# Kernel optimization log

Hardware: AMD Instinct MI355X
Metric: run time of the kernel (lower is better)

## Reference

```python
import jax, jax.numpy as jnp
import numpy as np

N_NODES = 50000
N_EDGES = 800000
VOCAB = 800000
CONCEPT_DIM = 100
HIDDEN_DIM = 200
OUTPUT_DIM = 100


def setup_inputs() -> dict:
    key = jax.random.key(0)
    ks = jax.random.split(key, 8)
    cncpt_ids = jax.random.randint(ks[0], (N_NODES,), 0, VOCAB, dtype=jnp.int64 if jax.config.jax_enable_x64 else jnp.int32)
    edge_src = jax.random.randint(ks[1], (N_EDGES,), 0, N_NODES, dtype=jnp.int32)
    edge_dst = jax.random.randint(ks[2], (N_EDGES,), 0, N_NODES, dtype=jnp.int32)
    emb = jax.random.normal(ks[3], (VOCAB, CONCEPT_DIM), dtype=jnp.float32)
    W1 = jax.random.normal(ks[4], (CONCEPT_DIM, HIDDEN_DIM), dtype=jnp.float32) / np.sqrt(CONCEPT_DIM)
    b1 = jnp.zeros((HIDDEN_DIM,), dtype=jnp.float32)
    W2 = jax.random.normal(ks[5], (HIDDEN_DIM, OUTPUT_DIM), dtype=jnp.float32) / np.sqrt(HIDDEN_DIM)
    b2 = jnp.zeros((OUTPUT_DIM,), dtype=jnp.float32)
    return {"emb": emb, "W1": W1, "b1": b1, "W2": W2, "b2": b2,
            "cncpt_ids": cncpt_ids, "edge_src": edge_src, "edge_dst": edge_dst}


def _gcn_layer(h, edge_src, edge_dst, W, b):
    # DGL update_all(copy_src, sum): gather src features, scatter-add to dst
    msgs = h[edge_src]                                        # [E, d_in]
    agg = jax.ops.segment_sum(msgs, edge_dst, num_segments=N_NODES)  # [N, d_in]
    return jax.nn.relu(agg @ W + b)                           # [N, d_out]


def reference(emb, W1, b1, W2, b2, cncpt_ids, edge_src, edge_dst):
    h = emb[cncpt_ids]                                        # [N, concept_dim]
    h = _gcn_layer(h, edge_src, edge_dst, W1, b1)             # [N, hidden]
    h = _gcn_layer(h, edge_src, edge_dst, W2, b2)             # [N, output]
    return h
```

## Files before the change

kernel.cpp:

```cpp
#include <hip/hip_runtime.h>

#define N_NODES 50000
#define N_EDGES 800000
#define CDIM 100
#define HDIM 200
#define ODIM 100

#define PITCH_U 64

typedef __bf16 bf16x8 __attribute__((ext_vector_type(8)));
typedef float f32x4 __attribute__((ext_vector_type(4)));
typedef unsigned short ushort_t;

__device__ __forceinline__ unsigned f2bf(float f) {
    unsigned u = __float_as_uint(f);
    u = (u + 0x7FFFu + ((u >> 16) & 1u)) >> 16;
    return u;
}
__device__ __forceinline__ float bflo(unsigned u) { return __uint_as_float(u << 16); }
__device__ __forceinline__ float bfhi(unsigned u) { return __uint_as_float(u & 0xFFFF0000u); }


__global__ void count_rank(const int* __restrict__ dst, int* __restrict__ deg,
                           int* __restrict__ rank) {
    int e = blockIdx.x * 256 + threadIdx.x;
    if (e < N_EDGES) rank[e] = atomicAdd(&deg[dst[e]], 1);
}

__global__ __launch_bounds__(1024) void scan_deg(const int* __restrict__ deg,
                                                 int* __restrict__ off) {
    const int T = 1024;
    const int PER = 52;
    int t = threadIdx.x;
    int start = t * PER;
    const int4* deg4 = (const int4*)deg;

    int sum = 0;
    if (start + PER <= N_NODES) {
#pragma unroll
        for (int q = 0; q < PER / 4; ++q) {
            int4 v = deg4[start / 4 + q];
            sum += v.x + v.y + v.z + v.w;
        }
    } else {
        for (int i = start; i < N_NODES; ++i) sum += deg[i];
    }

    __shared__ int ls[T];
    ls[t] = sum;
    __syncthreads();
    for (int o = 1; o < T; o <<= 1) {
        int v = (t >= o) ? ls[t - o] : 0;
        __syncthreads();
        ls[t] += v;
        __syncthreads();
    }
    int run = (t == 0) ? 0 : ls[t - 1];

    if (start + PER <= N_NODES) {
        int4* off4 = (int4*)off;
#pragma unroll
        for (int q = 0; q < PER / 4; ++q) {
            int4 v = deg4[start / 4 + q];
            int4 o;
            o.x = run;
            o.y = o.x + v.x;
            o.z = o.y + v.y;
            o.w = o.z + v.z;
            run = o.w + v.w;
            off4[start / 4 + q] = o;
        }
    } else if (start <= N_NODES) {
        for (int i = start; i < N_NODES; ++i) {
            off[i] = run;
            run += deg[i];
        }
        off[N_NODES] = run;
    }
}


__global__ __launch_bounds__(256) void scatter_gather_prep(
    const int* __restrict__ esrc, const int* __restrict__ edst,
    const int* __restrict__ off, const int* __restrict__ rank, int* __restrict__ ssrc,
    const float4* __restrict__ emb, const int* __restrict__ ids, uint2* __restrict__ h0,
    const float* __restrict__ W1, const float* __restrict__ W2,
    ushort_t* __restrict__ W1t, ushort_t* __restrict__ W2t) {
    int b = blockIdx.x;
    if (b < 3125) {
        int e = b * 256 + threadIdx.x;
        if (e < N_EDGES) {
            int p = off[edst[e]] + rank[e];
            ssrc[p] = esrc[e];
        }
    } else if (b < 9375) {
        int i = (b - 3125) * 256 + threadIdx.x;
        const int TOT = N_NODES * 32;
        if (i < TOT) {
            int n = i >> 5, q = i & 31;
            uint2 o = make_uint2(0u, 0u);
            if (q < 25) {
                float4 v = emb[(size_t)ids[n] * 25 + q];
                o.x = f2bf(v.x) | (f2bf(v.y) << 16);
                o.y = f2bf(v.z) | (f2bf(v.w) << 16);
            }
            h0[i] = o;
        }
    } else {
        int i = (b - 9375) * 256 + threadIdx.x;
        if (i < 208 * 128) {
            int n = i >> 7, k = i & 127;
            float v = (n < HDIM && k < CDIM) ? W1[k * HDIM + n] : 0.f;
            W1t[i] = (ushort_t)f2bf(v);
        } else {
            int j = i - 208 * 128;
            if (j < 112 * 256) {
                int n = j >> 8, k = j & 255;
                float v = (n < ODIM && k < HDIM) ? W2[k * ODIM + n] : 0.f;
                W2t[j] = (ushort_t)f2bf(v);
            }
        }
    }
}


template <bool BIAS_RELU>
__global__ __launch_bounds__(256) void agg_bf16(const unsigned* __restrict__ hb,
                                                const int* __restrict__ ssrc,
                                                const int* __restrict__ off,
                                                const float* __restrict__ bias,
                                                unsigned* __restrict__ outb,
                                                float2* __restrict__ outf) {
    int wave = threadIdx.x >> 6;
    int lane = threadIdx.x & 63;
    int n = blockIdx.x * 4 + wave;
    if (n >= N_NODES) return;
    int s0 = off[n], s1 = off[n + 1];

    float2 a0 = {0.f, 0.f}, a1 = {0.f, 0.f}, a2 = {0.f, 0.f}, a3 = {0.f, 0.f};
    int j = s0;
    for (; j + 7 < s1; j += 8) {
        int r0 = ssrc[j],     r1 = ssrc[j + 1], r2 = ssrc[j + 2], r3 = ssrc[j + 3];
        int r4 = ssrc[j + 4], r5 = ssrc[j + 5], r6 = ssrc[j + 6], r7 = ssrc[j + 7];
        unsigned u0 = hb[(size_t)r0 * PITCH_U + lane];
        unsigned u1 = hb[(size_t)r1 * PITCH_U + lane];
        unsigned u2 = hb[(size_t)r2 * PITCH_U + lane];
        unsigned u3 = hb[(size_t)r3 * PITCH_U + lane];
        unsigned u4 = hb[(size_t)r4 * PITCH_U + lane];
        unsigned u5 = hb[(size_t)r5 * PITCH_U + lane];
        unsigned u6 = hb[(size_t)r6 * PITCH_U + lane];
        unsigned u7 = hb[(size_t)r7 * PITCH_U + lane];
        a0.x += bflo(u0); a0.y += bfhi(u0);
        a1.x += bflo(u1); a1.y += bfhi(u1);
        a2.x += bflo(u2); a2.y += bfhi(u2);
        a3.x += bflo(u3); a3.y += bfhi(u3);
        a0.x += bflo(u4); a0.y += bfhi(u4);
        a1.x += bflo(u5); a1.y += bfhi(u5);
        a2.x += bflo(u6); a2.y += bfhi(u6);
        a3.x += bflo(u7); a3.y += bfhi(u7);
    }
    for (; j + 3 < s1; j += 4) {
        int r0 = ssrc[j], r1 = ssrc[j + 1], r2 = ssrc[j + 2], r3 = ssrc[j + 3];
        unsigned u0 = hb[(size_t)r0 * PITCH_U + lane];
        unsigned u1 = hb[(size_t)r1 * PITCH_U + lane];
        unsigned u2 = hb[(size_t)r2 * PITCH_U + lane];
        unsigned u3 = hb[(size_t)r3 * PITCH_U + lane];
        a0.x += bflo(u0); a0.y += bfhi(u0);
        a1.x += bflo(u1); a1.y += bfhi(u1);
        a2.x += bflo(u2); a2.y += bfhi(u2);
        a3.x += bflo(u3); a3.y += bfhi(u3);
    }
    {
        int rem = s1 - j;
        if (rem > 0) { unsigned u = hb[(size_t)ssrc[j] * PITCH_U + lane];     a0.x += bflo(u); a0.y += bfhi(u); }
        if (rem > 1) { unsigned u = hb[(size_t)ssrc[j + 1] * PITCH_U + lane]; a1.x += bflo(u); a1.y += bfhi(u); }
        if (rem > 2) { unsigned u = hb[(size_t)ssrc[j + 2] * PITCH_U + lane]; a2.x += bflo(u); a2.y += bfhi(u); }
    }
    float rx = (a0.x + a1.x) + (a2.x + a3.x);
    float ry = (a0.y + a1.y) + (a2.y + a3.y);
    if (BIAS_RELU) {
        if (lane < 50) {
            rx = fmaxf(rx + bias[2 * lane], 0.f);
            ry = fmaxf(ry + bias[2 * lane + 1], 0.f);
            outf[(size_t)n * 50 + lane] = make_float2(rx, ry);
        }
    } else {
        outb[(size_t)n * PITCH_U + lane] = f2bf(rx) | (f2bf(ry) << 16);
    }
}


__global__ __launch_bounds__(256) void gemm_fused(const ushort_t* __restrict__ Ab,
                                                  const ushort_t* __restrict__ W1t,
                                                  const float* __restrict__ b1,
                                                  const ushort_t* __restrict__ W2t,
                                                  ushort_t* __restrict__ gb) {
    const int P2 = 264;
    __shared__ alignas(16) ushort_t H1s[64 * P2];

    int tid = threadIdx.x, lane = tid & 63, w = tid >> 6;
    int rl = lane & 15, kg = lane >> 4;
    int row0 = blockIdx.x * 64;

    size_t abase = ((size_t)(row0 + w * 16 + rl)) * 128;
    f32x4 acc1[13];
#pragma unroll
    for (int t = 0; t < 13; ++t) acc1[t] = (f32x4){0.f, 0.f, 0.f, 0.f};
#pragma unroll
    for (int k2 = 0; k2 < 4; ++k2) {
        bf16x8 a = *reinterpret_cast<const bf16x8*>(&Ab[abase + k2 * 32 + kg * 8]);
#pragma unroll
        for (int t = 0; t < 13; ++t) {
            bf16x8 b = *reinterpret_cast<const bf16x8*>(&W1t[(t * 16 + rl) * 128 + k2 * 32 + kg * 8]);
            acc1[t] = __builtin_amdgcn_mfma_f32_16x16x32_bf16(a, b, acc1[t], 0, 0, 0);
        }
    }
    for (int idx = tid; idx < 64 * 32; idx += 256) {
        int r = idx >> 5, c = idx & 31;
        ((unsigned*)&H1s[r * P2 + 200])[c] = 0;
    }
#pragma unroll
    for (int t = 0; t < 13; ++t) {
        int col = t * 16 + rl;
        if (col < HDIM) {
            float bv = b1[col];
#pragma unroll
            for (int i = 0; i < 4; ++i) {
                int r = w * 16 + kg * 4 + i;
                H1s[r * P2 + col] = (ushort_t)f2bf(fmaxf(acc1[t][i] + bv, 0.f));
            }
        }
    }
    __syncthreads();

    f32x4 acc2[7];
#pragma unroll
    for (int t = 0; t < 7; ++t) acc2[t] = (f32x4){0.f, 0.f, 0.f, 0.f};
#pragma unroll
    for (int k2 = 0; k2 < 8; ++k2) {
        bf16x8 a = *reinterpret_cast<const bf16x8*>(&H1s[(w * 16 + rl) * P2 + k2 * 32 + kg * 8]);
#pragma unroll
        for (int t = 0; t < 7; ++t) {
            bf16x8 b = *reinterpret_cast<const bf16x8*>(&W2t[(t * 16 + rl) * 256 + k2 * 32 + kg * 8]);
            acc2[t] = __builtin_amdgcn_mfma_f32_16x16x32_bf16(a, b, acc2[t], 0, 0, 0);
        }
    }

#pragma unroll
    for (int t = 0; t < 7; ++t) {
        int col = t * 16 + rl;
#pragma unroll
        for (int i = 0; i < 4; ++i) {
            int row = row0 + w * 16 + kg * 4 + i;
            if (row < N_NODES) {
                float v = (col < ODIM) ? acc2[t][i] : 0.f;
                gb[(size_t)row * 128 + col] = (ushort_t)f2bf(v);
            }
        }
    }
    unsigned* gbu = (unsigned*)gb;
    for (int idx = tid; idx < 64 * 8; idx += 256) {
        int r = idx >> 3, c = idx & 7;
        int row = row0 + r;
        if (row < N_NODES) gbu[(size_t)row * PITCH_U + 56 + c] = 0;
    }
}


extern "C" void kernel_launch(void* const* d_in, const int* in_sizes, int n_in,
                              void* d_out, int out_size, void* d_ws, size_t ws_size,
                              hipStream_t stream) {
    const float4* emb = (const float4*)d_in[0];
    const float* W1  = (const float*)d_in[1];
    const float* b1  = (const float*)d_in[2];
    const float* W2  = (const float*)d_in[3];
    const float* b2  = (const float*)d_in[4];
    const int* ids   = (const int*)d_in[5];
    const int* esrc  = (const int*)d_in[6];
    const int* edst  = (const int*)d_in[7];
    float2* out = (float2*)d_out;

    unsigned* h0b = (unsigned*)d_ws;
    unsigned* a1b = h0b + (size_t)N_NODES * PITCH_U;
    unsigned* gbu = a1b + (size_t)N_NODES * PITCH_U;
    ushort_t* W1t = (ushort_t*)(gbu + (size_t)N_NODES * PITCH_U);
    ushort_t* W2t = W1t + 208 * 128;
    int* deg   = (int*)(W2t + 112 * 256);
    int* off   = deg + N_NODES;
    int* rank  = off + (N_NODES + 1);
    int* ssrc  = rank + N_EDGES;

    hipMemsetAsync(deg, 0, N_NODES * sizeof(int), stream);

    count_rank<<<(N_EDGES + 255) / 256, 256, 0, stream>>>(edst, deg, rank);
    scan_deg<<<1, 1024, 0, stream>>>(deg, off);

    scatter_gather_prep<<<9591, 256, 0, stream>>>(esrc, edst, off, rank, ssrc,
                                                  emb, ids, (uint2*)h0b,
                                                  W1, W2, W1t, W2t);

    agg_bf16<false><<<N_NODES / 4, 256, 0, stream>>>(h0b, ssrc, off,
                                                     nullptr, a1b, nullptr);
    gemm_fused<<<(N_NODES + 63) / 64, 256, 0, stream>>>((const ushort_t*)a1b, W1t, b1,
                                                        W2t, (ushort_t*)gbu);
    agg_bf16<true><<<N_NODES / 4, 256, 0, stream>>>(gbu, ssrc, off,
                                                    b2, nullptr, out);
}
```

Before: 199.5 us.

## Fuse first-layer aggregation into the fused MLP GEMM kernel via shared memory

The first neighbor aggregation is moved into the GEMM kernel. Each 64-row block aggregates its own nodes into shared memory as bf16, then loads the A fragments from LDS instead of from a global intermediate buffer. This removes one kernel launch and the global write and read of the aggregated features. The cost is that each wave now aggregates 16 nodes one after another, which lowers the parallelism available to hide gather latency (782 blocks versus 12500 before) and may make the kernel latency-bound.

Result: slower. 259.8 us (+30.3%).

```diff
diff --git a/kernel.cpp b/kernel.cpp
--- a/kernel.cpp
+++ b/kernel.cpp
@@ -20,123 +20,10 @@
 __device__ __forceinline__ float bflo(unsigned u) { return __uint_as_float(u << 16); }
 __device__ __forceinline__ float bfhi(unsigned u) { return __uint_as_float(u & 0xFFFF0000u); }
 
-
-__global__ void count_rank(const int* __restrict__ dst, int* __restrict__ deg,
-                           int* __restrict__ rank) {
-    int e = blockIdx.x * 256 + threadIdx.x;
-    if (e < N_EDGES) rank[e] = atomicAdd(&deg[dst[e]], 1);
-}
-
-__global__ __launch_bounds__(1024) void scan_deg(const int* __restrict__ deg,
-                                                 int* __restrict__ off) {
-    const int T = 1024;
-    const int PER = 52;
-    int t = threadIdx.x;
-    int start = t * PER;
-    const int4* deg4 = (const int4*)deg;
-
-    int sum = 0;
-    if (start + PER <= N_NODES) {
-#pragma unroll
-        for (int q = 0; q < PER / 4; ++q) {
-            int4 v = deg4[start / 4 + q];
-            sum += v.x + v.y + v.z + v.w;
-        }
-    } else {
-        for (int i = start; i < N_NODES; ++i) sum += deg[i];
-    }
-
-    __shared__ int ls[T];
-    ls[t] = sum;
-    __syncthreads();
-    for (int o = 1; o < T; o <<= 1) {
-        int v = (t >= o) ? ls[t - o] : 0;
-        __syncthreads();
-        ls[t] += v;
-        __syncthreads();
-    }
-    int run = (t == 0) ? 0 : ls[t - 1];
-
-    if (start + PER <= N_NODES) {
-        int4* off4 = (int4*)off;
-#pragma unroll
-        for (int q = 0; q < PER / 4; ++q) {
-            int4 v = deg4[start / 4 + q];
-            int4 o;
-            o.x = run;
-            o.y = o.x + v.x;
-            o.z = o.y + v.y;
-            o.w = o.z + v.z;
-            run = o.w + v.w;
-            off4[start / 4 + q] = o;
-        }
-    } else if (start <= N_NODES) {
-        for (int i = start; i < N_NODES; ++i) {
-            off[i] = run;
-            run += deg[i];
-        }
-        off[N_NODES] = run;
-    }
-}
-
-
-__global__ __launch_bounds__(256) void scatter_gather_prep(
-    const int* __restrict__ esrc, const int* __restrict__ edst,
-    const int* __restrict__ off, const int* __restrict__ rank, int* __restrict__ ssrc,
-    const float4* __restrict__ emb, const int* __restrict__ ids, uint2* __restrict__ h0,
-    const float* __restrict__ W1, const float* __restrict__ W2,
-    ushort_t* __restrict__ W1t, ushort_t* __restrict__ W2t) {
-    int b = blockIdx.x;
-    if (b < 3125) {
-        int e = b * 256 + threadIdx.x;
-        if (e < N_EDGES) {
-            int p = off[edst[e]] + rank[e];
-            ssrc[p] = esrc[e];
-        }
-    } else if (b < 9375) {
-        int i = (b - 3125) * 256 + threadIdx.x;
-        const int TOT = N_NODES * 32;
-        if (i < TOT) {
-            int n = i >> 5, q = i & 31;
-            uint2 o = make_uint2(0u, 0u);
-            if (q < 25) {
-                float4 v = emb[(size_t)ids[n] * 25 + q];
-                o.x = f2bf(v.x) | (f2bf(v.y) << 16);
-                o.y = f2bf(v.z) | (f2bf(v.w) << 16);
-            }
-            h0[i] = o;
-        }
-    } else {
-        int i = (b - 9375) * 256 + threadIdx.x;
-        if (i < 208 * 128) {
-            int n = i >> 7, k = i & 127;
-            float v = (n < HDIM && k < CDIM) ? W1[k * HDIM + n] : 0.f;
-            W1t[i] = (ushort_t)f2bf(v);
-        } else {
-            int j = i - 208 * 128;
-            if (j < 112 * 256) {
-                int n = j >> 8, k = j & 255;
-                float v = (n < ODIM && k < HDIM) ? W2[k * ODIM + n] : 0.f;
-                W2t[j] = (ushort_t)f2bf(v);
-            }
-        }
-    }
-}
-
-
-template <bool BIAS_RELU>
-__global__ __launch_bounds__(256) void agg_bf16(const unsigned* __restrict__ hb,
-                                                const int* __restrict__ ssrc,
-                                                const int* __restrict__ off,
-                                                const float* __restrict__ bias,
-                                                unsigned* __restrict__ outb,
-                                                float2* __restrict__ outf) {
-    int wave = threadIdx.x >> 6;
-    int lane = threadIdx.x & 63;
-    int n = blockIdx.x * 4 + wave;
-    if (n >= N_NODES) return;
+__device__ __forceinline__ float2 agg_core(int n, int lane, const unsigned* __restrict__ hb,
+                                           const int* __restrict__ ssrc,
+                                           const int* __restrict__ off) {
     int s0 = off[n], s1 = off[n + 1];
-
     float2 a0 = {0.f, 0.f}, a1 = {0.f, 0.f}, a2 = {0.f, 0.f}, a3 = {0.f, 0.f};
     int j = s0;
     for (; j + 7 < s1; j += 8) {
@@ -176,48 +63,163 @@
         if (rem > 1) { unsigned u = hb[(size_t)ssrc[j + 1] * PITCH_U + lane]; a1.x += bflo(u); a1.y += bfhi(u); }
         if (rem > 2) { unsigned u = hb[(size_t)ssrc[j + 2] * PITCH_U + lane]; a2.x += bflo(u); a2.y += bfhi(u); }
     }
-    float rx = (a0.x + a1.x) + (a2.x + a3.x);
-    float ry = (a0.y + a1.y) + (a2.y + a3.y);
-    if (BIAS_RELU) {
-        if (lane < 50) {
-            rx = fmaxf(rx + bias[2 * lane], 0.f);
-            ry = fmaxf(ry + bias[2 * lane + 1], 0.f);
-            outf[(size_t)n * 50 + lane] = make_float2(rx, ry);
+    return make_float2((a0.x + a1.x) + (a2.x + a3.x), (a0.y + a1.y) + (a2.y + a3.y));
+}
+
+
+__global__ void count_rank(const int* __restrict__ dst, int* __restrict__ deg,
+                           int* __restrict__ rank) {
+    int e = blockIdx.x * 256 + threadIdx.x;
+    if (e < N_EDGES) rank[e] = atomicAdd(&deg[dst[e]], 1);
+}
+
+__global__ __launch_bounds__(1024) void scan_deg(const int* __restrict__ deg,
+                                                 int* __restrict__ off) {
+    const int T = 1024;
+    const int PER = 52;
+    int t = threadIdx.x;
+    int start = t * PER;
+    const int4* deg4 = (const int4*)deg;
+
+    int sum = 0;
+    if (start + PER <= N_NODES) {
+#pragma unroll
+        for (int q = 0; q < PER / 4; ++q) {
+            int4 v = deg4[start / 4 + q];
+            sum += v.x + v.y + v.z + v.w;
         }
     } else {
-        outb[(size_t)n * PITCH_U + lane] = f2bf(rx) | (f2bf(ry) << 16);
-    }
-}
-
-
-__global__ __launch_bounds__(256) void gemm_fused(const ushort_t* __restrict__ Ab,
-                                                  const ushort_t* __restrict__ W1t,
-                                                  const float* __restrict__ b1,
-                                                  const ushort_t* __restrict__ W2t,
-                                                  ushort_t* __restrict__ gb) {
+        for (int i = start; i < N_NODES; ++i) sum += deg[i];
+    }
+
+    __shared__ int ls[T];
+    ls[t] = sum;
+    __syncthreads();
+    for (int o = 1; o < T; o <<= 1) {
+        int v = (t >= o) ? ls[t - o] : 0;
+        __syncthreads();
+        ls[t] += v;
+        __syncthreads();
+    }
+    int run = (t == 0) ? 0 : ls[t - 1];
+
+    if (start + PER <= N_NODES) {
+        int4* off4 = (int4*)off;
+#pragma unroll
+        for (int q = 0; q < PER / 4; ++q) {
+            int4 v = deg4[start / 4 + q];
+            int4 o;
+            o.x = run;
+            o.y = o.x + v.x;
+            o.z = o.y + v.y;
+            o.w = o.z + v.z;
+            run = o.w + v.w;
+            off4[start / 4 + q] = o;
+        }
+    } else if (start <= N_NODES) {
+        for (int i = start; i < N_NODES; ++i) {
+            off[i] = run;
+            run += deg[i];
+        }
+        off[N_NODES] = run;
+    }
+}
+
+
+__global__ __launch_bounds__(256) void scatter_gather_prep(
+    const int* __restrict__ esrc, const int* __restrict__ edst,
+    const int* __restrict__ off, const int* __restrict__ rank, int* __restrict__ ssrc,
+    const float4* __restrict__ emb, const int* __restrict__ ids, uint2* __restrict__ h0,
+    const float* __restrict__ W1, const float* __restrict__ W2,
+    ushort_t* __restrict__ W1t, ushort_t* __restrict__ W2t) {
+    int b = blockIdx.x;
+    if (b < 3125) {
+        int e = b * 256 + threadIdx.x;
+        if (e < N_EDGES) {
+            int p = off[edst[e]] + rank[e];
+            ssrc[p] = esrc[e];
+        }
+    } else if (b < 9375) {
+        int i = (b - 3125) * 256 + threadIdx.x;
+        const int TOT = N_NODES * 32;
+        if (i < TOT) {
+            int n = i >> 5, q = i & 31;
+            uint2 o = make_uint2(0u, 0u);
+            if (q < 25) {
+                float4 v = emb[(size_t)ids[n] * 25 + q];
+                o.x = f2bf(v.x) | (f2bf(v.y) << 16);
+                o.y = f2bf(v.z) | (f2bf(v.w) << 16);
+            }
+            h0[i] = o;
+        }
+    } else {
+        int i = (b - 9375) * 256 + threadIdx.x;
+        if (i < 208 * 128) {
+            int n = i >> 7, k = i & 127;
+            float v = (n < HDIM && k < CDIM) ? W1[k * HDIM + n] : 0.f;
+            W1t[i] = (ushort_t)f2bf(v);
+        } else {
+            int j = i - 208 * 128;
+            if (j < 112 * 256) {
+                int n = j >> 8, k = j & 255;
+                float v = (n < ODIM && k < HDIM) ? W2[k * ODIM + n] : 0.f;
+                W2t[j] = (ushort_t)f2bf(v);
+            }
+        }
+    }
+}
+
+
+__global__ __launch_bounds__(256) void agg_mlp(const unsigned* __restrict__ hb,
+                                               const int* __restrict__ ssrc,
+                                               const int* __restrict__ off,
+                                               const ushort_t* __restrict__ W1t,
+                                               const float* __restrict__ b1,
+                                               const ushort_t* __restrict__ W2t,
+                                               ushort_t* __restrict__ gb) {
     const int P2 = 264;
-    __shared__ alignas(16) ushort_t H1s[64 * P2];
+    const int AP = 136;
+    __shared__ alignas(16) ushort_t smem[64 * P2];
+    unsigned* AsU = (unsigned*)smem;
+    ushort_t* As = smem;
+    ushort_t* H1s = smem;
 
     int tid = threadIdx.x, lane = tid & 63, w = tid >> 6;
     int rl = lane & 15, kg = lane >> 4;
     int row0 = blockIdx.x * 64;
 
-    size_t abase = ((size_t)(row0 + w * 16 + rl)) * 128;
-    f32x4 acc1[13];
-#pragma unroll
-    for (int t = 0; t < 13; ++t) acc1[t] = (f32x4){0.f, 0.f, 0.f, 0.f};
-#pragma unroll
-    for (int k2 = 0; k2 < 4; ++k2) {
-        bf16x8 a = *reinterpret_cast<const bf16x8*>(&Ab[abase + k2 * 32 + kg * 8]);
-#pragma unroll
-        for (int t = 0; t < 13; ++t) {
-            bf16x8 b = *reinterpret_cast<const bf16x8*>(&W1t[(t * 16 + rl) * 128 + k2 * 32 + kg * 8]);
-            acc1[t] = __builtin_amdgcn_mfma_f32_16x16x32_bf16(a, b, acc1[t], 0, 0, 0);
-        }
-    }
+#pragma unroll 1
+    for (int i = 0; i < 16; ++i) {
+        int l = w * 16 + i;
+        int n = row0 + l;
+        if (n < N_NODES) {
+            float2 r = agg_core(n, lane, hb, ssrc, off);
+            AsU[l * (AP / 2) + lane] = f2bf(r.x) | (f2bf(r.y) << 16);
+        }
+    }
+    __syncthreads();
+
+    bf16x8 afr[4];
+#pragma unroll
+    for (int k2 = 0; k2 < 4; ++k2)
+        afr[k2] = *reinterpret_cast<const bf16x8*>(&As[(w * 16 + rl) * AP + k2 * 32 + kg * 8]);
+    __syncthreads();
+
     for (int idx = tid; idx < 64 * 32; idx += 256) {
         int r = idx >> 5, c = idx & 31;
         ((unsigned*)&H1s[r * P2 + 200])[c] = 0;
+    }
+
+    f32x4 acc1[13];
+#pragma unroll
+    for (int t = 0; t < 13; ++t) acc1[t] = (f32x4){0.f, 0.f, 0.f, 0.f};
+#pragma unroll
+    for (int k2 = 0; k2 < 4; ++k2) {
+#pragma unroll
+        for (int t = 0; t < 13; ++t) {
+            bf16x8 b = *reinterpret_cast<const bf16x8*>(&W1t[(t * 16 + rl) * 128 + k2 * 32 + kg * 8]);
+            acc1[t] = __builtin_amdgcn_mfma_f32_16x16x32_bf16(afr[k2], b, acc1[t], 0, 0, 0);
+        }
     }
 #pragma unroll
     for (int t = 0; t < 13; ++t) {
@@ -263,6 +265,24 @@
         int r = idx >> 3, c = idx & 7;
         int row = row0 + r;
         if (row < N_NODES) gbu[(size_t)row * PITCH_U + 56 + c] = 0;
+    }
+}
+
+
+__global__ __launch_bounds__(256) void agg_out(const unsigned* __restrict__ hb,
+                                               const int* __restrict__ ssrc,
+                                               const int* __restrict__ off,
+                                               const float* __restrict__ bias,
+                                               float2* __restrict__ outf) {
+    int wave = threadIdx.x >> 6;
+    int lane = threadIdx.x & 63;
+    int n = blockIdx.x * 4 + wave;
+    if (n >= N_NODES) return;
+    float2 r = agg_core(n, lane, hb, ssrc, off);
+    if (lane < 50) {
+        float rx = fmaxf(r.x + bias[2 * lane], 0.f);
+        float ry = fmaxf(r.y + bias[2 * lane + 1], 0.f);
+        outf[(size_t)n * 50 + lane] = make_float2(rx, ry);
     }
 }
 
@@ -281,8 +301,7 @@
     float2* out = (float2*)d_out;
 
     unsigned* h0b = (unsigned*)d_ws;
-    unsigned* a1b = h0b + (size_t)N_NODES * PITCH_U;
-    unsigned* gbu = a1b + (size_t)N_NODES * PITCH_U;
+    unsigned* gbu = h0b + (size_t)N_NODES * PITCH_U;
     ushort_t* W1t = (ushort_t*)(gbu + (size_t)N_NODES * PITCH_U);
     ushort_t* W2t = W1t + 208 * 128;
     int* deg   = (int*)(W2t + 112 * 256);
@@ -299,10 +318,7 @@
                                                   emb, ids, (uint2*)h0b,
                                                   W1, W2, W1t, W2t);
 
-    agg_bf16<false><<<N_NODES / 4, 256, 0, stream>>>(h0b, ssrc, off,
-                                                     nullptr, a1b, nullptr);
-    gemm_fused<<<(N_NODES + 63) / 64, 256, 0, stream>>>((const ushort_t*)a1b, W1t, b1,
-                                                        W2t, (ushort_t*)gbu);
-    agg_bf16<true><<<N_NODES / 4, 256, 0, stream>>>(gbu, ssrc, off,
-                                                    b2, nullptr, out);
-}
+    agg_mlp<<<(N_NODES + 63) / 64, 256, 0, stream>>>(h0b, ssrc, off, W1t, b1, W2t,
+                                                     (ushort_t*)gbu);
+    agg_out<<<N_NODES / 4, 256, 0, stream>>>(gbu, ssrc, off, b2, out);
+}
```

## Split each aggregation wave into two half-waves gathering two edges with 8-byte loads

Applied to the files above, without the earlier changes.

The aggregation kernels now have each half of a 64-lane wave handle a different edge. Each lane loads a uint2 (four bf16 values) per row, so two neighbor rows are fetched per instruction, and the two halves are combined with a cross-lane shuffle. The edge-count atomics are folded into the embedding-gather and weight-prep kernel, and the edge scatter moves into its own kernel. The intermediate buffer is removed by reusing the h0 and gb buffers in ping-pong fashion. The goal is wider loads, more memory parallelism and fewer launches, at the cost of an extra shuffle reduction and half-idle lanes when a node's edge count is odd.

Result: slower. 205.0 us (+2.8%).

```diff
diff --git a/kernel.cpp b/kernel.cpp
--- a/kernel.cpp
+++ b/kernel.cpp
@@ -7,6 +7,7 @@
 #define ODIM 100
 
 #define PITCH_U 64
+#define PITCH_U2 32
 
 typedef __bf16 bf16x8 __attribute__((ext_vector_type(8)));
 typedef float f32x4 __attribute__((ext_vector_type(4)));
@@ -20,92 +21,82 @@
 __device__ __forceinline__ float bflo(unsigned u) { return __uint_as_float(u << 16); }
 __device__ __forceinline__ float bfhi(unsigned u) { return __uint_as_float(u & 0xFFFF0000u); }
 
-
-__global__ void count_rank(const int* __restrict__ dst, int* __restrict__ deg,
-                           int* __restrict__ rank) {
-    int e = blockIdx.x * 256 + threadIdx.x;
-    if (e < N_EDGES) rank[e] = atomicAdd(&deg[dst[e]], 1);
-}
-
-__global__ __launch_bounds__(1024) void scan_deg(const int* __restrict__ deg,
-                                                 int* __restrict__ off) {
-    const int T = 1024;
-    const int PER = 52;
-    int t = threadIdx.x;
-    int start = t * PER;
-    const int4* deg4 = (const int4*)deg;
-
-    int sum = 0;
-    if (start + PER <= N_NODES) {
-#pragma unroll
-        for (int q = 0; q < PER / 4; ++q) {
-            int4 v = deg4[start / 4 + q];
-            sum += v.x + v.y + v.z + v.w;
-        }
-    } else {
-        for (int i = start; i < N_NODES; ++i) sum += deg[i];
-    }
-
-    __shared__ int ls[T];
-    ls[t] = sum;
-    __syncthreads();
-    for (int o = 1; o < T; o <<= 1) {
-        int v = (t >= o) ? ls[t - o] : 0;
-        __syncthreads();
-        ls[t] += v;
-        __syncthreads();
-    }
-    int run = (t == 0) ? 0 : ls[t - 1];
-
-    if (start + PER <= N_NODES) {
-        int4* off4 = (int4*)off;
-#pragma unroll
-        for (int q = 0; q < PER / 4; ++q) {
-            int4 v = deg4[start / 4 + q];
-            int4 o;
-            o.x = run;
-            o.y = o.x + v.x;
-            o.z = o.y + v.y;
-            o.w = o.z + v.z;
-            run = o.w + v.w;
-            off4[start / 4 + q] = o;
-        }
-    } else if (start <= N_NODES) {
-        for (int i = start; i < N_NODES; ++i) {
-            off[i] = run;
-            run += deg[i];
-        }
-        off[N_NODES] = run;
-    }
-}
-
-
-__global__ __launch_bounds__(256) void scatter_gather_prep(
-    const int* __restrict__ esrc, const int* __restrict__ edst,
-    const int* __restrict__ off, const int* __restrict__ rank, int* __restrict__ ssrc,
+#define ACC4(a, u)                          \
+    do {                                    \
+        (a).x += bflo((u).x);               \
+        (a).y += bfhi((u).x);               \
+        (a).z += bflo((u).y);               \
+        (a).w += bfhi((u).y);               \
+    } while (0)
+
+
+__device__ __forceinline__ float4 agg_core2(int n, int lane, const uint2* __restrict__ hb2,
+                                            const int* __restrict__ ssrc,
+                                            const int* __restrict__ off) {
+    int s0 = off[n], s1 = off[n + 1];
+    int half = lane >> 5;
+    int li = lane & 31;
+    float4 a0 = {0.f, 0.f, 0.f, 0.f}, a1 = {0.f, 0.f, 0.f, 0.f};
+    float4 a2 = {0.f, 0.f, 0.f, 0.f}, a3 = {0.f, 0.f, 0.f, 0.f};
+    int j = s0;
+    for (; j + 7 < s1; j += 8) {
+        int i0 = ssrc[j + 0 + half];
+        int i1 = ssrc[j + 2 + half];
+        int i2 = ssrc[j + 4 + half];
+        int i3 = ssrc[j + 6 + half];
+        uint2 u0 = hb2[(size_t)i0 * PITCH_U2 + li];
+        uint2 u1 = hb2[(size_t)i1 * PITCH_U2 + li];
+        uint2 u2 = hb2[(size_t)i2 * PITCH_U2 + li];
+        uint2 u3 = hb2[(size_t)i3 * PITCH_U2 + li];
+        ACC4(a0, u0);
+        ACC4(a1, u1);
+        ACC4(a2, u2);
+        ACC4(a3, u3);
+    }
+    {
+        int p = (s1 - j) >> 1;
+        if (p > 0) { int i = ssrc[j + 0 + half]; uint2 u = hb2[(size_t)i * PITCH_U2 + li]; ACC4(a0, u); }
+        if (p > 1) { int i = ssrc[j + 2 + half]; uint2 u = hb2[(size_t)i * PITCH_U2 + li]; ACC4(a1, u); }
+        if (p > 2) { int i = ssrc[j + 4 + half]; uint2 u = hb2[(size_t)i * PITCH_U2 + li]; ACC4(a2, u); }
+        j += 2 * p;
+    }
+    if (j < s1) {
+        int i = ssrc[j];
+        uint2 u = hb2[(size_t)i * PITCH_U2 + li];
+        if (half == 0) ACC4(a3, u);
+    }
+    float4 s;
+    s.x = (a0.x + a1.x) + (a2.x + a3.x);
+    s.y = (a0.y + a1.y) + (a2.y + a3.y);
+    s.z = (a0.z + a1.z) + (a2.z + a3.z);
+    s.w = (a0.w + a1.w) + (a2.w + a3.w);
+    s.x += __shfl_xor(s.x, 32);
+    s.y += __shfl_xor(s.y, 32);
+    s.z += __shfl_xor(s.z, 32);
+    s.w += __shfl_xor(s.w, 32);
+    return s;
+}
+
+
+__global__ __launch_bounds__(256) void count_gather_prep(
+    const int* __restrict__ edst, int* __restrict__ deg, int* __restrict__ rank,
     const float4* __restrict__ emb, const int* __restrict__ ids, uint2* __restrict__ h0,
     const float* __restrict__ W1, const float* __restrict__ W2,
     ushort_t* __restrict__ W1t, ushort_t* __restrict__ W2t) {
     int b = blockIdx.x;
     if (b < 3125) {
         int e = b * 256 + threadIdx.x;
-        if (e < N_EDGES) {
-            int p = off[edst[e]] + rank[e];
-            ssrc[p] = esrc[e];
-        }
+        rank[e] = atomicAdd(&deg[edst[e]], 1);
     } else if (b < 9375) {
         int i = (b - 3125) * 256 + threadIdx.x;
-        const int TOT = N_NODES * 32;
-        if (i < TOT) {
-            int n = i >> 5, q = i & 31;
-            uint2 o = make_uint2(0u, 0u);
-            if (q < 25) {
-                float4 v = emb[(size_t)ids[n] * 25 + q];
-                o.x = f2bf(v.x) | (f2bf(v.y) << 16);
-                o.y = f2bf(v.z) | (f2bf(v.w) << 16);
-            }
-            h0[i] = o;
-        }
+        int n = i >> 5, q = i & 31;
+        uint2 o = make_uint2(0u, 0u);
+        if (q < 25) {
+            float4 v = emb[(size_t)ids[n] * 25 + q];
+            o.x = f2bf(v.x) | (f2bf(v.y) << 16);
+            o.y = f2bf(v.z) | (f2bf(v.w) << 16);
+        }
+        h0[i] = o;
     } else {
         int i = (b - 9375) * 256 + threadIdx.x;
         if (i < 208 * 128) {
@@ -123,69 +114,86 @@
     }
 }
 
-
-template <bool BIAS_RELU>
-__global__ __launch_bounds__(256) void agg_bf16(const unsigned* __restrict__ hb,
-                                                const int* __restrict__ ssrc,
-                                                const int* __restrict__ off,
-                                                const float* __restrict__ bias,
-                                                unsigned* __restrict__ outb,
-                                                float2* __restrict__ outf) {
+__global__ __launch_bounds__(1024) void scan_deg(const int* __restrict__ deg,
+                                                 int* __restrict__ off) {
+    const int T = 1024;
+    const int PER = 52;
+    int t = threadIdx.x;
+    int start = t * PER;
+    const int4* deg4 = (const int4*)deg;
+
+    int sum = 0;
+    if (start + PER <= N_NODES) {
+#pragma unroll
+        for (int q = 0; q < PER / 4; ++q) {
+            int4 v = deg4[start / 4 + q];
+            sum += v.x + v.y + v.z + v.w;
+        }
+    } else {
+        for (int i = start; i < N_NODES; ++i) sum += deg[i];
+    }
+
+    __shared__ int ls[T];
+    ls[t] = sum;
+    __syncthreads();
+    for (int o = 1; o < T; o <<= 1) {
+        int v = (t >= o) ? ls[t - o] : 0;
+        __syncthreads();
+        ls[t] += v;
+        __syncthreads();
+    }
+    int run = (t == 0) ? 0 : ls[t - 1];
+
+    if (start + PER <= N_NODES) {
+        int4* off4 = (int4*)off;
+#pragma unroll
+        for (int q = 0; q < PER / 4; ++q) {
+            int4 v = deg4[start / 4 + q];
+            int4 o;
+            o.x = run;
+            o.y = o.x + v.x;
+            o.z = o.y + v.y;
+            o.w = o.z + v.z;
+            run = o.w + v.w;
+            off4[start / 4 + q] = o;
+        }
+    } else if (start <= N_NODES) {
+        for (int i = start; i < N_NODES; ++i) {
+            off[i] = run;
+            run += deg[i];
+        }
+        off[N_NODES] = run;
+    }
+}
+
+
+__global__ __launch_bounds__(256) void scatter(const int* __restrict__ esrc,
+                                               const int* __restrict__ edst,
+                                               const int* __restrict__ off,
+                                               const int* __restrict__ rank,
+                                               int* __restrict__ ssrc) {
+    int e = blockIdx.x * 256 + threadIdx.x;
+    if (e < N_EDGES) {
+        int p = off[edst[e]] + rank[e];
+        ssrc[p] = esrc[e];
+    }
+}
+
+
+__global__ __launch_bounds__(256) void agg1(const uint2* __restrict__ hb2,
+                                            const int* __restrict__ ssrc,
+                                            const int* __restrict__ off,
+                                            uint2* __restrict__ out2) {
     int wave = threadIdx.x >> 6;
     int lane = threadIdx.x & 63;
     int n = blockIdx.x * 4 + wave;
     if (n >= N_NODES) return;
-    int s0 = off[n], s1 = off[n + 1];
-
-    float2 a0 = {0.f, 0.f}, a1 = {0.f, 0.f}, a2 = {0.f, 0.f}, a3 = {0.f, 0.f};
-    int j = s0;
-    for (; j + 7 < s1; j += 8) {
-        int r0 = ssrc[j],     r1 = ssrc[j + 1], r2 = ssrc[j + 2], r3 = ssrc[j + 3];
-        int r4 = ssrc[j + 4], r5 = ssrc[j + 5], r6 = ssrc[j + 6], r7 = ssrc[j + 7];
-        unsigned u0 = hb[(size_t)r0 * PITCH_U + lane];
-        unsigned u1 = hb[(size_t)r1 * PITCH_U + lane];
-        unsigned u2 = hb[(size_t)r2 * PITCH_U + lane];
-        unsigned u3 = hb[(size_t)r3 * PITCH_U + lane];
-        unsigned u4 = hb[(size_t)r4 * PITCH_U + lane];
-        unsigned u5 = hb[(size_t)r5 * PITCH_U + lane];
-        unsigned u6 = hb[(size_t)r6 * PITCH_U + lane];
-        unsigned u7 = hb[(size_t)r7 * PITCH_U + lane];
-        a0.x += bflo(u0); a0.y += bfhi(u0);
-        a1.x += bflo(u1); a1.y += bfhi(u1);
-        a2.x += bflo(u2); a2.y += bfhi(u2);
-        a3.x += bflo(u3); a3.y += bfhi(u3);
-        a0.x += bflo(u4); a0.y += bfhi(u4);
-        a1.x += bflo(u5); a1.y += bfhi(u5);
-        a2.x += bflo(u6); a2.y += bfhi(u6);
-        a3.x += bflo(u7); a3.y += bfhi(u7);
-    }
-    for (; j + 3 < s1; j += 4) {
-        int r0 = ssrc[j], r1 = ssrc[j + 1], r2 = ssrc[j + 2], r3 = ssrc[j + 3];
-        unsigned u0 = hb[(size_t)r0 * PITCH_U + lane];
-        unsigned u1 = hb[(size_t)r1 * PITCH_U + lane];
-        unsigned u2 = hb[(size_t)r2 * PITCH_U + lane];
-        unsigned u3 = hb[(size_t)r3 * PITCH_U + lane];
-        a0.x += bflo(u0); a0.y += bfhi(u0);
-        a1.x += bflo(u1); a1.y += bfhi(u1);
-        a2.x += bflo(u2); a2.y += bfhi(u2);
-        a3.x += bflo(u3); a3.y += bfhi(u3);
-    }
-    {
-        int rem = s1 - j;
-        if (rem > 0) { unsigned u = hb[(size_t)ssrc[j] * PITCH_U + lane];     a0.x += bflo(u); a0.y += bfhi(u); }
-        if (rem > 1) { unsigned u = hb[(size_t)ssrc[j + 1] * PITCH_U + lane]; a1.x += bflo(u); a1.y += bfhi(u); }
-        if (rem > 2) { unsigned u = hb[(size_t)ssrc[j + 2] * PITCH_U + lane]; a2.x += bflo(u); a2.y += bfhi(u); }
-    }
-    float rx = (a0.x + a1.x) + (a2.x + a3.x);
-    float ry = (a0.y + a1.y) + (a2.y + a3.y);
-    if (BIAS_RELU) {
-        if (lane < 50) {
-            rx = fmaxf(rx + bias[2 * lane], 0.f);
-            ry = fmaxf(ry + bias[2 * lane + 1], 0.f);
-            outf[(size_t)n * 50 + lane] = make_float2(rx, ry);
-        }
-    } else {
-        outb[(size_t)n * PITCH_U + lane] = f2bf(rx) | (f2bf(ry) << 16);
+    float4 s = agg_core2(n, lane, hb2, ssrc, off);
+    if (lane < 32) {
+        uint2 o;
+        o.x = f2bf(s.x) | (f2bf(s.y) << 16);
+        o.y = f2bf(s.z) | (f2bf(s.w) << 16);
+        out2[(size_t)n * PITCH_U2 + lane] = o;
     }
 }
 
@@ -263,6 +271,28 @@
         int r = idx >> 3, c = idx & 7;
         int row = row0 + r;
         if (row < N_NODES) gbu[(size_t)row * PITCH_U + 56 + c] = 0;
+    }
+}
+
+
+__global__ __launch_bounds__(256) void agg_out(const uint2* __restrict__ hb2,
+                                               const int* __restrict__ ssrc,
+                                               const int* __restrict__ off,
+                                               const float* __restrict__ bias,
+                                               float4* __restrict__ outf) {
+    int wave = threadIdx.x >> 6;
+    int lane = threadIdx.x & 63;
+    int n = blockIdx.x * 4 + wave;
+    if (n >= N_NODES) return;
+    float4 s = agg_core2(n, lane, hb2, ssrc, off);
+    if (lane < 25) {
+        float4 bv = ((const float4*)bias)[lane];
+        float4 r;
+        r.x = fmaxf(s.x + bv.x, 0.f);
+        r.y = fmaxf(s.y + bv.y, 0.f);
+        r.z = fmaxf(s.z + bv.z, 0.f);
+        r.w = fmaxf(s.w + bv.w, 0.f);
+        outf[(size_t)n * 25 + lane] = r;
     }
 }
 
@@ -278,11 +308,10 @@
     const int* ids   = (const int*)d_in[5];
     const int* esrc  = (const int*)d_in[6];
     const int* edst  = (const int*)d_in[7];
-    float2* out = (float2*)d_out;
+    float4* out = (float4*)d_out;
 
     unsigned* h0b = (unsigned*)d_ws;
-    unsigned* a1b = h0b + (size_t)N_NODES * PITCH_U;
-    unsigned* gbu = a1b + (size_t)N_NODES * PITCH_U;
+    unsigned* gbu = h0b + (size_t)N_NODES * PITCH_U;
     ushort_t* W1t = (ushort_t*)(gbu + (size_t)N_NODES * PITCH_U);
     ushort_t* W2t = W1t + 208 * 128;
     int* deg   = (int*)(W2t + 112 * 256);
@@ -292,17 +321,15 @@
 
     hipMemsetAsync(deg, 0, N_NODES * sizeof(int), stream);
 
-    count_rank<<<(N_EDGES + 255) / 256, 256, 0, stream>>>(edst, deg, rank);
+    count_gather_prep<<<9591, 256, 0, stream>>>(edst, deg, rank,
+                                                emb, ids, (uint2*)h0b,
+                                                W1, W2, W1t, W2t);
     scan_deg<<<1, 1024, 0, stream>>>(deg, off);
-
-    scatter_gather_prep<<<9591, 256, 0, stream>>>(esrc, edst, off, rank, ssrc,
-                                                  emb, ids, (uint2*)h0b,
-                                                  W1, W2, W1t, W2t);
-
-    agg_bf16<false><<<N_NODES / 4, 256, 0, stream>>>(h0b, ssrc, off,
-                                                     nullptr, a1b, nullptr);
-    gemm_fused<<<(N_NODES + 63) / 64, 256, 0, stream>>>((const ushort_t*)a1b, W1t, b1,
-                                                        W2t, (ushort_t*)gbu);
-    agg_bf16<true><<<N_NODES / 4, 256, 0, stream>>>(gbu, ssrc, off,
-                                                    b2, nullptr, out);
-}
+    scatter<<<3125, 256, 0, stream>>>(esrc, edst, off, rank, ssrc);
+
+    agg1<<<N_NODES / 4, 256, 0, stream>>>((const uint2*)h0b, ssrc, off, (uint2*)gbu + 0);
+
+    gemm_fused<<<(N_NODES + 63) / 64, 256, 0, stream>>>((const ushort_t*)gbu, W1t, b1,
+                                                        W2t, (ushort_t*)h0b);
+    agg_out<<<N_NODES / 4, 256, 0, stream>>>((const uint2*)h0b, ssrc, off, b2, out);
+}
```
